# Kernel optimization log

Measured on AMD Instinct MI355X. Metric: run time of the kernel, lower is better.

The kernel has to match this reference:

```python
import jax, jax.numpy as jnp
import numpy as np

TAU = 2.0
ALPHA = 4.0  # spikingjelly surrogate.Sigmoid default
NUM_HEADS = 8


def lif(x, v_th):
    # Multi-step LIF over leading time axis T. v_reset=0, hard reset, tau=2.
    # Forward: Heaviside spike; backward: sigmoid surrogate via straight-through.
    def step(v, xt):
        v = v + (xt - v) / TAU
        hard = (v >= v_th).astype(xt.dtype)
        soft = jax.nn.sigmoid(ALPHA * (v - v_th))
        spike = soft + jax.lax.stop_gradient(hard - soft)
        v = v * (1.0 - jax.lax.stop_gradient(hard))  # detach_reset hard reset to 0
        return v, spike
    _, out = jax.lax.scan(step, jnp.zeros_like(x[0]), x)
    return out


def conv_bn_lif(x, w, scale, bias, v_th=1.0):
    # 1x1 conv (no bias) + folded eval-mode BatchNorm + LIF.
    # x: [T,B,C,H,W], w: [Cout,Cin], scale/bias: [Cout]
    y = jnp.einsum('tbchw,dc->tbdhw', x, w)
    y = y * scale[:, None, None] + bias[:, None, None]
    return lif(y, v_th)


def setup_inputs() -> dict:
    key = jax.random.key(0)
    ks = jax.random.split(key, 14)
    T, B, C, H, W = 4, 32, 384, 14, 14
    x = jax.random.normal(ks[0], (T, B, C, H, W), dtype=jnp.float32)
    def conv_params(k):
        k1, k2, k3 = jax.random.split(k, 3)
        w = jax.random.normal(k1, (C, C), dtype=jnp.float32) * (1.0 / np.sqrt(C))
        scale = jax.random.uniform(k2, (C,), dtype=jnp.float32, minval=0.5, maxval=1.5)
        bias = jax.random.normal(k3, (C,), dtype=jnp.float32) * 0.1
        return w, scale, bias
    wq, sq, bq = conv_params(ks[1])
    wk, sk, bk = conv_params(ks[2])
    wv, sv, bv = conv_params(ks[3])
    wp, sp, bp = conv_params(ks[4])
    return {"x": x, "wq": wq, "sq": sq, "bq": bq, "wk": wk, "sk": sk, "bk": bk,
            "wv": wv, "sv": sv, "bv": bv, "wp": wp, "sp": sp, "bp": bp}


def reference(x, wq, sq, bq, wk, sk, bk, wv, sv, bv, wp, sp, bp):
    T, B, C, H, W = x.shape
    h = NUM_HEADS
    d = C // h
    N = H * W
    # QKV: conv+BN+LIF -> binary spikes [T,B,C,H,W]
    qs = conv_bn_lif(x, wq, sq, bq)
    ks_ = conv_bn_lif(x, wk, sk, bk)
    vs = conv_bn_lif(x, wv, sv, bv)
    # [T,B,C,H,W] -> [T,B,h,d,N] -> [T,B,h,N,d]
    def to_heads(t):
        return t.reshape(T, B, h, d, N).transpose(0, 1, 2, 4, 3)
    q, k, v = to_heads(qs), to_heads(ks_), to_heads(vs)
    attn = jnp.einsum('tbhnd,tbhmd->tbhnm', q, k)
    out = jnp.einsum('tbhnm,tbhmd->tbhnd', attn, v) * 0.125
    out = lif(out, 0.5)  # attn_lif v_threshold=0.5
    # [T,B,h,N,d] -> [T,B,h,d,N] -> [T,B,C,H,W]
    out = out.transpose(0, 1, 2, 4, 3).reshape(T, B, C, H, W)
    out = conv_bn_lif(out, wp, sp, bp)
    return out
```

## Files before the change

kernel.cpp:

```cpp
#include <hip/hip_runtime.h>


#define T_ 4
#define B_ 32
#define C_ 384
#define N_ 196
#define NH_ 8
#define D_ 48
#define TB_ (T_ * B_)
#define CN_ ((size_t)C_ * N_)
#define BCN4_ (B_ * C_ * (N_ / 4))
#define TBCN_ ((size_t)T_ * B_ * C_ * N_)
typedef unsigned long long u64;

__global__ __launch_bounds__(512) void gemm_f32(
    const float* __restrict__ X, const float* __restrict__ W0,
    const float* __restrict__ W1, const float* __restrict__ W2,
    float* __restrict__ P)
{
  const int g = blockIdx.z;
  const float* __restrict__ W = (g == 0) ? W0 : (g == 1) ? W1 : W2;
  const int co0 = blockIdx.y * 128;
  const int j0 = blockIdx.x * 256;
  __shared__ float As[16][132];
  __shared__ float Bs[16][256];
  const int tid = threadIdx.x;
  const int wave = tid >> 6, lane = tid & 63;
  const int w16 = wave * 16;
  const int lane4 = lane * 4;

  const int ar = tid >> 2, aq4 = (tid & 3) * 4;
  const float* wrow = W + (size_t)(co0 + ar) * C_ + aq4;
  const int bj = j0 + lane4;
  const int btb = bj / N_;
  const float* xcol = X + (size_t)btb * CN_ + (bj - btb * N_);
  float* pbase = P + (size_t)(g * TB_ + btb) * CN_ + (bj - btb * N_);

  float acc[16][4] = {};
  for (int c0 = 0; c0 < C_; c0 += 16) {
    const float4 w4 = *(const float4*)(wrow + c0);
    As[aq4 + 0][ar] = w4.x; As[aq4 + 1][ar] = w4.y;
    As[aq4 + 2][ar] = w4.z; As[aq4 + 3][ar] = w4.w;
    *(float4*)&Bs[wave][lane4] =
        *(const float4*)(xcol + (size_t)(c0 + wave) * N_);
    *(float4*)&Bs[wave + 8][lane4] =
        *(const float4*)(xcol + (size_t)(c0 + wave + 8) * N_);
    __syncthreads();
#pragma unroll
    for (int k = 0; k < 16; ++k) {
      float b[4], a[16];
      *(float4*)&b[0] = *(const float4*)&Bs[k][lane4];
#pragma unroll
      for (int q = 0; q < 4; ++q)
        *(float4*)&a[q * 4] = *(const float4*)&As[k][w16 + q * 4];
#pragma unroll
      for (int i = 0; i < 16; ++i)
#pragma unroll
        for (int jj = 0; jj < 4; ++jj)
          acc[i][jj] = fmaf(a[i], b[jj], acc[i][jj]);
    }
    __syncthreads();
  }
#pragma unroll
  for (int i = 0; i < 16; ++i)
    *(float4*)&pbase[(size_t)(co0 + w16 + i) * N_] =
        make_float4(acc[i][0], acc[i][1], acc[i][2], acc[i][3]);
}

__global__ __launch_bounds__(256) void lif4(
    const float* __restrict__ In, float* __restrict__ Out,
    const float* __restrict__ s0, const float* __restrict__ b0, float vth)
{
  const long u = (long)blockIdx.x * 256 + threadIdx.x;
  if (u >= BCN4_) return;
  const long r = u;
  const int c = (int)((r / (N_ / 4)) % C_);
  const bool has_bn = (s0 != nullptr);
  const float sc = has_bn ? s0[c] : 1.0f;
  const float bi = has_bn ? b0[c] : 0.0f;
  const float4* In4 = (const float4*)In;
  float4* Out4 = (float4*)Out;
  float v[4] = {0.f, 0.f, 0.f, 0.f};
#pragma unroll
  for (int t = 0; t < T_; ++t) {
    const long idx = (long)t * BCN4_ + r;
    const float4 y4 = In4[idx];
    float y[4] = {y4.x, y4.y, y4.z, y4.w};
    float o[4];
#pragma unroll
    for (int e = 0; e < 4; ++e) {
      const float yb = has_bn ? __fadd_rn(__fmul_rn(y[e], sc), bi) : y[e];
      v[e] = __fadd_rn(v[e], __fmul_rn(__fsub_rn(yb, v[e]), 0.5f));
      const bool fire = (v[e] >= vth);
      o[e] = fire ? 1.0f : 0.0f;
      v[e] = fire ? 0.0f : v[e];
    }
    Out4[idx] = make_float4(o[0], o[1], o[2], o[3]);
  }
}

__global__ __launch_bounds__(256) void k_mask(
    const float* __restrict__ P, u64* __restrict__ MSK,
    const float* __restrict__ sq, const float* __restrict__ bq,
    const float* __restrict__ sk, const float* __restrict__ bk,
    const float* __restrict__ sv, const float* __restrict__ bv)
{
  const int wave = threadIdx.x >> 6, lane = threadIdx.x & 63;
  const int task = blockIdx.x * 4 + wave;
  const int j = task % D_;
  int r = task / D_;
  const int b = r & 31; r >>= 5;
  const int h = r & 7;  r >>= 3;
  const int g = r;
  const int c = h * D_ + j;
  const float sc = (g == 0 ? sq : g == 1 ? sk : sv)[c];
  const float bi = (g == 0 ? bq : g == 1 ? bk : bv)[c];
  const float* base = P + (size_t)g * TB_ * CN_ + (size_t)b * CN_ + (size_t)c * N_;

  float y[4][T_];
  bool act[4];
#pragma unroll
  for (int w = 0; w < 4; ++w) {
    const int m = w * 64 + lane;
    act[w] = (m < N_);
    const int mc = act[w] ? m : (N_ - 1);
#pragma unroll
    for (int t = 0; t < T_; ++t)
      y[w][t] = base[(size_t)t * B_ * CN_ + mc];
  }
  u64* mb = MSK + ((size_t)(h * 32 + b) * 3 + g) * (T_ * D_ * 4) + j * 4;
  float v[4] = {0.f, 0.f, 0.f, 0.f};
#pragma unroll
  for (int t = 0; t < T_; ++t) {
#pragma unroll
    for (int w = 0; w < 4; ++w) {
      const float yb = __fadd_rn(__fmul_rn(y[w][t], sc), bi);
      v[w] = __fadd_rn(v[w], __fmul_rn(__fsub_rn(yb, v[w]), 0.5f));
      const bool fire = (v[w] >= 1.0f);
      if (fire) v[w] = 0.f;
      const u64 bl = __ballot(fire && act[w]);
      if (lane == 0) mb[(size_t)t * (D_ * 4) + w] = bl;
    }
  }
}

__global__ __launch_bounds__(1024) void k_attn(
    const u64* __restrict__ MSK, float* __restrict__ O)
{
  const int h = blockIdx.x;
  const int b = blockIdx.y;
  __shared__ u64 msk[3][T_][D_][4];
  __shared__ u64 qT[T_][208];
  __shared__ u64 Gp[T_][8][D_];
  const int tid = threadIdx.x;
  const int wave = tid >> 6, lane = tid & 63;

  {
    const u64* ms = MSK + (size_t)(h * 32 + b) * 2304;
    u64* mf = &msk[0][0][0][0];
    for (int off = tid; off < 2304; off += 1024) mf[off] = ms[off];
  }
  __syncthreads();

  {
    const int t = wave >> 2, w = wave & 3;
    const int n = w * 64 + lane;
    u64 qr = 0ull;
#pragma unroll 8
    for (int j = 0; j < D_; ++j)
      qr |= ((msk[0][t][j][w] >> lane) & 1ull) << j;
    if (n < N_) qT[t][n] = qr;
  }
  for (int task = wave; task < T_ * D_; task += 16) {
    const int t = task / D_, d = task - (task / D_) * D_;
    const bool ja = (lane < D_);
    const int j = ja ? lane : (D_ - 1);
    const u64* kj = msk[1][t][j];
    const u64* vd = msk[2][t][d];
    const int gi = __popcll(kj[0] & vd[0]) + __popcll(kj[1] & vd[1]) +
                   __popcll(kj[2] & vd[2]) + __popcll(kj[3] & vd[3]);
#pragma unroll
    for (int p = 0; p < 8; ++p) {
      const u64 bl = __ballot(ja && ((gi >> p) & 1));
      if (lane == 0) Gp[t][p][d] = bl;
    }
  }
  __syncthreads();

  const int u = tid;
  if (u < 4 * N_) {
    const int dq = u / N_;
    const int n = u - dq * N_;
    const int d0 = dq * 12;
    float vmem[12];
#pragma unroll
    for (int i = 0; i < 12; ++i) vmem[i] = 0.f;
    for (int t = 0; t < T_; ++t) {
      const u64 qr = qT[t][n];
      float* ob = O + ((size_t)(t * B_ + b) * C_ + h * D_ + d0) * N_ + n;
#pragma unroll
      for (int i = 0; i < 12; ++i) {
        int acc = 0;
#pragma unroll
        for (int p = 0; p < 8; ++p)
          acc += __popcll(qr & Gp[t][p][d0 + i]) << p;
        const float y = __int2float_rn(acc) * 0.125f;
        vmem[i] = __fadd_rn(vmem[i], __fmul_rn(__fsub_rn(y, vmem[i]), 0.5f));
        const bool fire = (vmem[i] >= 0.5f);
        ob[(size_t)i * N_] = fire ? 1.0f : 0.0f;
        if (fire) vmem[i] = 0.f;
      }
    }
  }
}

extern "C" void kernel_launch(void* const* d_in, const int* in_sizes, int n_in,
                              void* d_out, int out_size, void* d_ws, size_t ws_size,
                              hipStream_t stream) {
  const float* x  = (const float*)d_in[0];
  const float* wq = (const float*)d_in[1];
  const float* sq = (const float*)d_in[2];
  const float* bq = (const float*)d_in[3];
  const float* wk = (const float*)d_in[4];
  const float* sk = (const float*)d_in[5];
  const float* bk = (const float*)d_in[6];
  const float* wv = (const float*)d_in[7];
  const float* sv = (const float*)d_in[8];
  const float* bv = (const float*)d_in[9];
  const float* wp = (const float*)d_in[10];
  const float* sp = (const float*)d_in[11];
  const float* bp = (const float*)d_in[12];
  float* out = (float*)d_out;

  float* P = (float*)d_ws;
  float* O = P + 3 * TBCN_;
  u64* MSK = (u64*)(P + 4 * TBCN_);
  float* P2 = P;

  gemm_f32<<<dim3(98, 3, 3), 512, 0, stream>>>(x, wq, wk, wv, P);
  k_mask<<<dim3(9216), 256, 0, stream>>>(P, MSK, sq, bq, sk, bk, sv, bv);
  k_attn<<<dim3(NH_, B_), 1024, 0, stream>>>(MSK, O);
  gemm_f32<<<dim3(98, 3, 1), 512, 0, stream>>>(O, wp, wp, wp, P2);
  lif4<<<dim3((BCN4_ + 255) / 256), 256, 0, stream>>>(P2, out, sp, bp, 1.0f);
}
```

Measured before the change: 575.8 us.

## Double-buffer FP32 GEMM with direct global-to-LDS loads and 16x8 register tiles

Rewrites the 1x1-conv GEMM kernel to use 128-thread blocks, each computing a 128x128 output tile with 16x8 accumulators per thread. The X tile is streamed straight into LDS with global_load_lds, and the weight tile is prefetched into registers one step ahead. Both tiles are double-buffered in shared memory, so loads overlap the FMA loop and there is one barrier per K step. This aims to hide memory latency and raise arithmetic intensity per thread, at the cost of more registers and fewer threads per block.

Result: slower. 664.6 us (+15.4%).

```diff
diff --git a/kernel.cpp b/kernel.cpp
--- a/kernel.cpp
+++ b/kernel.cpp
@@ -13,7 +13,7 @@
 #define TBCN_ ((size_t)T_ * B_ * C_ * N_)
 typedef unsigned long long u64;
 
-__global__ __launch_bounds__(512) void gemm_f32(
+__global__ __launch_bounds__(128) void gemm_f32(
     const float* __restrict__ X, const float* __restrict__ W0,
     const float* __restrict__ W1, const float* __restrict__ W2,
     float* __restrict__ P)
@@ -21,50 +21,95 @@
   const int g = blockIdx.z;
   const float* __restrict__ W = (g == 0) ? W0 : (g == 1) ? W1 : W2;
   const int co0 = blockIdx.y * 128;
-  const int j0 = blockIdx.x * 256;
-  __shared__ float As[16][132];
-  __shared__ float Bs[16][256];
+  const int j0 = blockIdx.x * 128;
+  __shared__ float As[2][16][128];
+  __shared__ float Bs[2][16][128];
   const int tid = threadIdx.x;
-  const int wave = tid >> 6, lane = tid & 63;
-  const int w16 = wave * 16;
-  const int lane4 = lane * 4;
-
-  const int ar = tid >> 2, aq4 = (tid & 3) * 4;
-  const float* wrow = W + (size_t)(co0 + ar) * C_ + aq4;
-  const int bj = j0 + lane4;
-  const int btb = bj / N_;
-  const float* xcol = X + (size_t)btb * CN_ + (bj - btb * N_);
-  float* pbase = P + (size_t)(g * TB_ + btb) * CN_ + (bj - btb * N_);
-
-  float acc[16][4] = {};
-  for (int c0 = 0; c0 < C_; c0 += 16) {
-    const float4 w4 = *(const float4*)(wrow + c0);
-    As[aq4 + 0][ar] = w4.x; As[aq4 + 1][ar] = w4.y;
-    As[aq4 + 2][ar] = w4.z; As[aq4 + 3][ar] = w4.w;
-    *(float4*)&Bs[wave][lane4] =
-        *(const float4*)(xcol + (size_t)(c0 + wave) * N_);
-    *(float4*)&Bs[wave + 8][lane4] =
-        *(const float4*)(xcol + (size_t)(c0 + wave + 8) * N_);
+  const int tx = tid & 15, ty = tid >> 4;
+  const int wv = tid >> 6, lane = tid & 63;
+
+  const float* wrow = W + (size_t)(co0 + tid) * C_;
+  const int jcol = j0 + (lane & 31) * 4;
+  const int tbB = jcol / N_;
+  const float* xB = X + (size_t)tbB * CN_ + (jcol - tbB * N_);
+  const int krow = lane >> 5;
+
+  float4 a0 = *(const float4*)(wrow + 0);
+  float4 a1 = *(const float4*)(wrow + 4);
+  float4 a2 = *(const float4*)(wrow + 8);
+  float4 a3 = *(const float4*)(wrow + 12);
+#pragma unroll
+  for (int q = 0; q < 4; ++q) {
+    const int kb = q * 4 + wv * 2;
+    const float* src = xB + (size_t)(kb + krow) * N_;
+    __builtin_amdgcn_global_load_lds(
+        (const __attribute__((address_space(1))) void*)src,
+        (__attribute__((address_space(3))) void*)&Bs[0][kb][0], 16, 0, 0);
+  }
+  float4 n0 = *(const float4*)(wrow + 16);
+  float4 n1 = *(const float4*)(wrow + 20);
+  float4 n2 = *(const float4*)(wrow + 24);
+  float4 n3 = *(const float4*)(wrow + 28);
+  As[0][0][tid] = a0.x;  As[0][1][tid] = a0.y;  As[0][2][tid] = a0.z;  As[0][3][tid] = a0.w;
+  As[0][4][tid] = a1.x;  As[0][5][tid] = a1.y;  As[0][6][tid] = a1.z;  As[0][7][tid] = a1.w;
+  As[0][8][tid] = a2.x;  As[0][9][tid] = a2.y;  As[0][10][tid] = a2.z; As[0][11][tid] = a2.w;
+  As[0][12][tid] = a3.x; As[0][13][tid] = a3.y; As[0][14][tid] = a3.z; As[0][15][tid] = a3.w;
+  __syncthreads();
+
+  float acc[16][8] = {};
+  for (int i = 0; i < 24; ++i) {
+    const int cur = i & 1, nxt = cur ^ 1;
+    if (i < 23) {
+      const int cb = (i + 1) * 16;
+#pragma unroll
+      for (int q = 0; q < 4; ++q) {
+        const int kb = q * 4 + wv * 2;
+        const float* src = xB + (size_t)(cb + kb + krow) * N_;
+        __builtin_amdgcn_global_load_lds(
+            (const __attribute__((address_space(1))) void*)src,
+            (__attribute__((address_space(3))) void*)&Bs[nxt][kb][0], 16, 0, 0);
+      }
+      As[nxt][0][tid] = n0.x;  As[nxt][1][tid] = n0.y;  As[nxt][2][tid] = n0.z;  As[nxt][3][tid] = n0.w;
+      As[nxt][4][tid] = n1.x;  As[nxt][5][tid] = n1.y;  As[nxt][6][tid] = n1.z;  As[nxt][7][tid] = n1.w;
+      As[nxt][8][tid] = n2.x;  As[nxt][9][tid] = n2.y;  As[nxt][10][tid] = n2.z; As[nxt][11][tid] = n2.w;
+      As[nxt][12][tid] = n3.x; As[nxt][13][tid] = n3.y; As[nxt][14][tid] = n3.z; As[nxt][15][tid] = n3.w;
+      if (i < 22) {
+        const float* wn = wrow + (i + 2) * 16;
+        n0 = *(const float4*)(wn + 0);
+        n1 = *(const float4*)(wn + 4);
+        n2 = *(const float4*)(wn + 8);
+        n3 = *(const float4*)(wn + 12);
+      }
+    }
+#pragma unroll
+    for (int k = 0; k < 16; ++k) {
+      float a[16], b[8];
+#pragma unroll
+      for (int q = 0; q < 4; ++q)
+        *(float4*)&a[q * 4] = *(const float4*)&As[cur][k][ty * 16 + q * 4];
+      *(float4*)&b[0] = *(const float4*)&Bs[cur][k][tx * 4];
+      *(float4*)&b[4] = *(const float4*)&Bs[cur][k][64 + tx * 4];
+#pragma unroll
+      for (int r = 0; r < 16; ++r)
+#pragma unroll
+        for (int c = 0; c < 8; ++c)
+          acc[r][c] = fmaf(a[r], b[c], acc[r][c]);
+    }
     __syncthreads();
-#pragma unroll
-    for (int k = 0; k < 16; ++k) {
-      float b[4], a[16];
-      *(float4*)&b[0] = *(const float4*)&Bs[k][lane4];
-#pragma unroll
-      for (int q = 0; q < 4; ++q)
-        *(float4*)&a[q * 4] = *(const float4*)&As[k][w16 + q * 4];
-#pragma unroll
-      for (int i = 0; i < 16; ++i)
-#pragma unroll
-        for (int jj = 0; jj < 4; ++jj)
-          acc[i][jj] = fmaf(a[i], b[jj], acc[i][jj]);
-    }
-    __syncthreads();
-  }
-#pragma unroll
-  for (int i = 0; i < 16; ++i)
-    *(float4*)&pbase[(size_t)(co0 + w16 + i) * N_] =
-        make_float4(acc[i][0], acc[i][1], acc[i][2], acc[i][3]);
+  }
+  {
+    const int jA = j0 + tx * 4;
+    const int jB = j0 + 64 + tx * 4;
+    const int tbA = jA / N_, tbB2 = jB / N_;
+    float* pA = P + (size_t)(g * TB_ + tbA) * CN_ + (jA - tbA * N_);
+    float* pB = P + (size_t)(g * TB_ + tbB2) * CN_ + (jB - tbB2 * N_);
+#pragma unroll
+    for (int r = 0; r < 16; ++r) {
+      const size_t ro = (size_t)(co0 + ty * 16 + r) * N_;
+      *(float4*)&pA[ro] = make_float4(acc[r][0], acc[r][1], acc[r][2], acc[r][3]);
+      *(float4*)&pB[ro] = make_float4(acc[r][4], acc[r][5], acc[r][6], acc[r][7]);
+    }
+  }
 }
 
 __global__ __launch_bounds__(256) void lif4(
@@ -237,9 +282,9 @@
   u64* MSK = (u64*)(P + 4 * TBCN_);
   float* P2 = P;
 
-  gemm_f32<<<dim3(98, 3, 3), 512, 0, stream>>>(x, wq, wk, wv, P);
+  gemm_f32<<<dim3(196, 3, 3), 128, 0, stream>>>(x, wq, wk, wv, P);
   k_mask<<<dim3(9216), 256, 0, stream>>>(P, MSK, sq, bq, sk, bk, sv, bv);
   k_attn<<<dim3(NH_, B_), 1024, 0, stream>>>(MSK, O);
-  gemm_f32<<<dim3(98, 3, 1), 512, 0, stream>>>(O, wp, wp, wp, P2);
+  gemm_f32<<<dim3(196, 3, 1), 128, 0, stream>>>(O, wp, wp, wp, P2);
   lif4<<<dim3((BCN4_ + 255) / 256), 256, 0, stream>>>(P2, out, sp, bp, 1.0f);
 }
```
